# Optimization experiments

Measured on AMD Instinct MI355X. Metric: run time of the kernel, lower is better.

## Reference

```python
import jax, jax.numpy as jnp
import numpy as np

N_NODES = 100000
N_EDGES = 3200000
D_FEAT = 64


def setup_inputs() -> dict:
    key = jax.random.key(0)
    k1, k2, k3, k4 = jax.random.split(key, 4)
    features = jax.random.normal(k1, (N_NODES, D_FEAT), dtype=jnp.float32)
    vals = jax.random.uniform(k2, (N_EDGES,), dtype=jnp.float32)  # Laplacian nonzero values (e.g. 1/sqrt(di*dj))
    rows = jax.random.randint(k3, (N_EDGES,), 0, N_NODES)
    cols = jax.random.randint(k4, (N_EDGES,), 0, N_NODES)
    return {"features": features, "vals": vals, "rows": rows, "cols": cols}


def reference(features, vals, rows, cols):
    # (L + I) @ features, with L given in COO (rows, cols, vals).
    # Gather source node features, scale by edge value, scatter-add to destination rows.
    msgs = vals[:, None] * features[cols]              # [E, d]
    agg = jax.ops.segment_sum(msgs, rows, num_segments=N_NODES)  # [N, d]
    # self-loop (identity sparse matrix) fused as a direct add
    return agg + features
```

## Files before the change

kernel.cpp:

```cpp
#include <hip/hip_runtime.h>
#include <hip/hip_bf16.h>
#include <hip/hip_fp16.h>

#define D 64
#define RB 200
#define NB_MAX 512
#define MAGIC 21474944u
#define SC_BLK 256
#define TILE_T 32
#define TILE (SC_BLK * TILE_T)

__device__ __forceinline__ int bucket_of(int r) {
    return (int)__umulhi((unsigned)r, MAGIC);
}

__global__ void k_hist(const int* __restrict__ rows, int* __restrict__ counts,
                       int E, int nb) {
    __shared__ int h[NB_MAX];
    for (int i = threadIdx.x; i < nb; i += blockDim.x) h[i] = 0;
    __syncthreads();
    int i = blockIdx.x * blockDim.x + threadIdx.x;
    int stride = gridDim.x * blockDim.x;
    for (; i < E; i += stride) atomicAdd(&h[bucket_of(rows[i])], 1);
    __syncthreads();
    for (int j = threadIdx.x; j < nb; j += blockDim.x)
        if (h[j]) atomicAdd(&counts[j], h[j]);
}

__global__ void k_scan(const int* __restrict__ counts, int* __restrict__ starts,
                       int* __restrict__ cursor, int nb) {
    __shared__ int lds[NB_MAX];
    int t = threadIdx.x;
    int v = (t < nb) ? counts[t] : 0;
    lds[t] = v;
    __syncthreads();
    for (int off = 1; off < NB_MAX; off <<= 1) {
        int x = (t >= off) ? lds[t - off] : 0;
        __syncthreads();
        lds[t] += x;
        __syncthreads();
    }
    if (t < nb) {
        int excl = lds[t] - v;
        starts[t] = excl;
        cursor[t] = excl;
        if (t == nb - 1) starts[nb] = lds[t];
    }
}

__global__ void __launch_bounds__(SC_BLK) k_scatter(
    const int* __restrict__ rows, const int* __restrict__ cols,
    const float* __restrict__ vals, int* __restrict__ cursor,
    unsigned long long* __restrict__ packed1, int E, int nb) {
    __shared__ int cnt[NB_MAX];
    __shared__ int bas[NB_MAX];
    __shared__ int cnt2[NB_MAX];
    int t = threadIdx.x;
    int tile = blockIdx.x * TILE;
    for (int i = t; i < nb; i += SC_BLK) { cnt[i] = 0; cnt2[i] = 0; }
    __syncthreads();

    int rk[TILE_T];
#pragma unroll
    for (int k = 0; k < TILE_T; ++k) {
        int e = tile + k * SC_BLK + t;
        rk[k] = (e < E) ? rows[e] : -1;
        if (rk[k] >= 0) atomicAdd(&cnt[bucket_of(rk[k])], 1);
    }
    __syncthreads();
    for (int i = t; i < nb; i += SC_BLK)
        if (cnt[i]) bas[i] = atomicAdd(&cursor[i], cnt[i]);
    __syncthreads();
#pragma unroll
    for (int k = 0; k < TILE_T; ++k) {
        int e = tile + k * SC_BLK + t;
        if (rk[k] >= 0) {
            int b = bucket_of(rk[k]);
            int slot = atomicAdd(&cnt2[b], 1);
            int pos = bas[b] + slot;
            int roff = rk[k] - b * RB;
            unsigned lo = ((unsigned)roff << 17) | (unsigned)cols[e];
            packed1[pos] =
                ((unsigned long long)__float_as_uint(vals[e]) << 32) | lo;
        }
    }
}

__global__ void __launch_bounds__(1024) k_sort(
    const unsigned long long* __restrict__ packed1, const int* __restrict__ starts,
    unsigned* __restrict__ packed2, int* __restrict__ rowptr, int N, int E) {
    __shared__ int rhist[RB];
    __shared__ int rcur[RB];
    __shared__ int sc[256];
    int b = blockIdx.x;
    int t = threadIdx.x;
    int s = starts[b];
    int e = starts[b + 1];

    for (int i = t; i < RB; i += 1024) rhist[i] = 0;
    __syncthreads();
    for (int i = s + t; i < e; i += 1024) {
        unsigned lo = (unsigned)packed1[i];
        atomicAdd(&rhist[(lo >> 17) & 0xFF], 1);
    }
    __syncthreads();
    if (t < 256) sc[t] = (t < RB) ? rhist[t] : 0;
    __syncthreads();
    for (int off = 1; off < 256; off <<= 1) {
        int x = (t < 256 && t >= off) ? sc[t - off] : 0;
        __syncthreads();
        if (t < 256) sc[t] += x;
        __syncthreads();
    }
    if (t < RB) rcur[t] = sc[t] - rhist[t];
    __syncthreads();

    int gbase = b * RB;
    int nr = N - gbase; if (nr > RB) nr = RB;
    if (t < nr) rowptr[gbase + t] = s + (sc[t] - rhist[t]);
    if (b == 0 && t == 0) rowptr[N] = E;

    for (int i = s + t; i < e; i += 1024) {
        unsigned long long dj = packed1[i];
        unsigned lo = (unsigned)dj;
        int ro = (int)((lo >> 17) & 0xFF);
        int slot = atomicAdd(&rcur[ro], 1);
        float v = __uint_as_float((unsigned)(dj >> 32));
        unsigned hb = (unsigned)__half_as_ushort(__float2half(v));
        packed2[s + slot] = (hb << 17) | (lo & 0x1FFFFu);
    }
}

__global__ void __launch_bounds__(256) k_spmm(
    const float* __restrict__ feat, const unsigned* __restrict__ packed2,
    const int* __restrict__ rowptr, float* __restrict__ out, int N) {
    int lane = threadIdx.x & 63;
    int wid = (int)(((long long)blockIdx.x * blockDim.x + threadIdx.x) >> 6);
    if (wid >= N) return;
    int s = rowptr[wid];
    int e = rowptr[wid + 1];

    float acc = feat[(size_t)wid * D + lane];
    int i = s;
    for (; i + 8 <= e; i += 8) {
        float g[8], vv[8];
#pragma unroll
        for (int u = 0; u < 8; ++u) {
            unsigned d = packed2[i + u];
            vv[u] = __half2float(__ushort_as_half((unsigned short)(d >> 17)));
            g[u] = feat[(size_t)(d & 0x1FFFFu) * D + lane];
        }
#pragma unroll
        for (int u = 0; u < 8; ++u) acc = fmaf(vv[u], g[u], acc);
    }
    for (; i < e; ++i) {
        unsigned d = packed2[i];
        float v = __half2float(__ushort_as_half((unsigned short)(d >> 17)));
        acc = fmaf(v, feat[(size_t)(d & 0x1FFFFu) * D + lane], acc);
    }
    out[(size_t)wid * D + lane] = acc;
}

__global__ void gp_init_kernel(const float4* __restrict__ feat, float4* __restrict__ out,
                               int n4) {
    int i = blockIdx.x * blockDim.x + threadIdx.x;
    int stride = gridDim.x * blockDim.x;
    for (; i < n4; i += stride) out[i] = feat[i];
}
__global__ void gp_edge_kernel(const float* __restrict__ feat, const float* __restrict__ vals,
                               const int* __restrict__ rows, const int* __restrict__ cols,
                               float* __restrict__ out, int n_edges) {
    int lane = threadIdx.x & 63;
    long long gtid = (long long)blockIdx.x * blockDim.x + threadIdx.x;
    int e = (int)(gtid >> 6);
    if (e >= n_edges) return;
    int r = rows[e];
    int c = cols[e];
    float v = vals[e];
    float x = feat[(long long)c * D + lane];
    unsafeAtomicAdd(&out[(long long)r * D + lane], v * x);
}

extern "C" void kernel_launch(void* const* d_in, const int* in_sizes, int n_in,
                              void* d_out, int out_size, void* d_ws, size_t ws_size,
                              hipStream_t stream) {
    const float* feat = (const float*)d_in[0];
    const float* vals = (const float*)d_in[1];
    const int* rows = (const int*)d_in[2];
    const int* cols = (const int*)d_in[3];
    float* out = (float*)d_out;

    int E = in_sizes[1];
    int N = out_size / D;
    int nb = (N + RB - 1) / RB;

    size_t off_rowptr = (size_t)E * 4;
    size_t off_counts = off_rowptr + (size_t)(N + 1) * 4;
    size_t off_starts = off_counts + (size_t)NB_MAX * 4;
    size_t off_cursor = off_starts + (size_t)(NB_MAX + 1) * 4;
    size_t needed = off_cursor + (size_t)NB_MAX * 4;
    bool out_fits = ((size_t)out_size * 4) >= ((size_t)E * 8);

    if (ws_size >= needed && nb <= NB_MAX && N < 131072 && out_fits) {
        char* ws = (char*)d_ws;
        unsigned* packed2 = (unsigned*)ws;
        int* rowptr = (int*)(ws + off_rowptr);
        int* counts = (int*)(ws + off_counts);
        int* starts = (int*)(ws + off_starts);
        int* cursor = (int*)(ws + off_cursor);
        unsigned long long* packed1 = (unsigned long long*)d_out;

        hipMemsetAsync(counts, 0, (size_t)nb * 4, stream);
        k_hist<<<256, 256, 0, stream>>>(rows, counts, E, nb);
        k_scan<<<1, NB_MAX, 0, stream>>>(counts, starts, cursor, nb);
        int gScat = (E + TILE - 1) / TILE;
        k_scatter<<<gScat, SC_BLK, 0, stream>>>(rows, cols, vals, cursor, packed1, E, nb);
        k_sort<<<nb, 1024, 0, stream>>>(packed1, starts, packed2, rowptr, N, E);
        long long tt = (long long)N * 64;
        k_spmm<<<(int)((tt + 255) / 256), 256, 0, stream>>>(feat, packed2, rowptr, out, N);
    } else {
        int n4 = out_size / 4;
        int grid = (n4 + 255) / 256;
        if (grid > 4096) grid = 4096;
        gp_init_kernel<<<grid, 256, 0, stream>>>((const float4*)feat, (float4*)out, n4);
        long long tthreads = (long long)E * 64;
        gp_edge_kernel<<<(int)((tthreads + 255) / 256), 256, 0, stream>>>(feat, vals, rows, cols,
                                                                          out, E);
    }
}
```

Before: 317.5 us.

## Stage bucket scatter through LDS for coalesced writes and vectorize histogram loads

The scatter kernel now sorts each 4096-edge tile by bucket in shared memory, using a local prefix scan, and then writes records out contiguously per bucket. Previously each thread scattered 8-byte records directly to random global slots. The change also vectorizes the row loads in the histogram and scatter kernels with int4/float4. It adds a block-level scan, more LDS use (about 48KB per block) and extra syncs, which may reduce occupancy.

```diff
diff --git a/kernel.cpp b/kernel.cpp
--- a/kernel.cpp
+++ b/kernel.cpp
@@ -6,9 +6,8 @@
 #define RB 200
 #define NB_MAX 512
 #define MAGIC 21474944u
-#define SC_BLK 256
-#define TILE_T 32
-#define TILE (SC_BLK * TILE_T)
+#define SC_TILE 4096
+#define SC_PT 16
 
 __device__ __forceinline__ int bucket_of(int r) {
     return (int)__umulhi((unsigned)r, MAGIC);
@@ -19,9 +18,19 @@
     __shared__ int h[NB_MAX];
     for (int i = threadIdx.x; i < nb; i += blockDim.x) h[i] = 0;
     __syncthreads();
+    int E4 = E >> 2;
     int i = blockIdx.x * blockDim.x + threadIdx.x;
     int stride = gridDim.x * blockDim.x;
-    for (; i < E; i += stride) atomicAdd(&h[bucket_of(rows[i])], 1);
+    const int4* rows4 = (const int4*)rows;
+    for (; i < E4; i += stride) {
+        int4 r4 = rows4[i];
+        atomicAdd(&h[bucket_of(r4.x)], 1);
+        atomicAdd(&h[bucket_of(r4.y)], 1);
+        atomicAdd(&h[bucket_of(r4.z)], 1);
+        atomicAdd(&h[bucket_of(r4.w)], 1);
+    }
+    int t0 = E4 * 4 + blockIdx.x * blockDim.x + threadIdx.x;
+    if (t0 < E) atomicAdd(&h[bucket_of(rows[t0])], 1);
     __syncthreads();
     for (int j = threadIdx.x; j < nb; j += blockDim.x)
         if (h[j]) atomicAdd(&counts[j], h[j]);
@@ -48,42 +57,107 @@
     }
 }
 
-__global__ void __launch_bounds__(SC_BLK) k_scatter(
+__global__ void __launch_bounds__(256) k_scatter2(
     const int* __restrict__ rows, const int* __restrict__ cols,
     const float* __restrict__ vals, int* __restrict__ cursor,
-    unsigned long long* __restrict__ packed1, int E, int nb) {
+    unsigned long long* __restrict__ packed1, int E) {
+    __shared__ unsigned long long recs[SC_TILE];
+    __shared__ int dsts[SC_TILE];
     __shared__ int cnt[NB_MAX];
+    __shared__ int tst[NB_MAX];
     __shared__ int bas[NB_MAX];
-    __shared__ int cnt2[NB_MAX];
+    __shared__ int cur[NB_MAX];
+
     int t = threadIdx.x;
-    int tile = blockIdx.x * TILE;
-    for (int i = t; i < nb; i += SC_BLK) { cnt[i] = 0; cnt2[i] = 0; }
-    __syncthreads();
-
-    int rk[TILE_T];
-#pragma unroll
-    for (int k = 0; k < TILE_T; ++k) {
-        int e = tile + k * SC_BLK + t;
-        rk[k] = (e < E) ? rows[e] : -1;
-        if (rk[k] >= 0) atomicAdd(&cnt[bucket_of(rk[k])], 1);
-    }
-    __syncthreads();
-    for (int i = t; i < nb; i += SC_BLK)
-        if (cnt[i]) bas[i] = atomicAdd(&cursor[i], cnt[i]);
-    __syncthreads();
-#pragma unroll
-    for (int k = 0; k < TILE_T; ++k) {
-        int e = tile + k * SC_BLK + t;
-        if (rk[k] >= 0) {
-            int b = bucket_of(rk[k]);
-            int slot = atomicAdd(&cnt2[b], 1);
-            int pos = bas[b] + slot;
-            int roff = rk[k] - b * RB;
-            unsigned lo = ((unsigned)roff << 17) | (unsigned)cols[e];
-            packed1[pos] =
-                ((unsigned long long)__float_as_uint(vals[e]) << 32) | lo;
-        }
-    }
+    int tile = blockIdx.x * SC_TILE;
+    int tile_n = E - tile; if (tile_n > SC_TILE) tile_n = SC_TILE;
+    bool full = (tile_n == SC_TILE);
+
+    cnt[t] = 0; cnt[t + 256] = 0;
+    __syncthreads();
+
+    int r[SC_PT];
+    int e0 = tile + t * SC_PT;
+    if (full) {
+        const int4* r4 = (const int4*)(rows + e0);
+#pragma unroll
+        for (int g = 0; g < 4; ++g) {
+            int4 rr = r4[g];
+            r[g * 4 + 0] = rr.x; r[g * 4 + 1] = rr.y;
+            r[g * 4 + 2] = rr.z; r[g * 4 + 3] = rr.w;
+        }
+#pragma unroll
+        for (int u = 0; u < SC_PT; ++u) atomicAdd(&cnt[bucket_of(r[u])], 1);
+    } else {
+#pragma unroll
+        for (int u = 0; u < SC_PT; ++u) {
+            int e = e0 + u;
+            r[u] = (e < E) ? rows[e] : -1;
+            if (r[u] >= 0) atomicAdd(&cnt[bucket_of(r[u])], 1);
+        }
+    }
+    __syncthreads();
+
+    {
+        int c0 = cnt[t], c1 = cnt[t + 256];
+        bas[t] = c0 ? atomicAdd(&cursor[t], c0) : 0;
+        bas[t + 256] = c1 ? atomicAdd(&cursor[t + 256], c1) : 0;
+        tst[t] = c0; tst[t + 256] = c1;
+    }
+    __syncthreads();
+    for (int off = 1; off < NB_MAX; off <<= 1) {
+        int v0 = (t >= off) ? tst[t - off] : 0;
+        int v1 = (t + 256 >= off) ? tst[t + 256 - off] : 0;
+        __syncthreads();
+        tst[t] += v0; tst[t + 256] += v1;
+        __syncthreads();
+    }
+    {
+        int e0_ = tst[t] - cnt[t];
+        int e1_ = tst[t + 256] - cnt[t + 256];
+        __syncthreads();
+        tst[t] = e0_; tst[t + 256] = e1_;
+        cur[t] = e0_; cur[t + 256] = e1_;
+    }
+    __syncthreads();
+
+    if (full) {
+        const int4* c4 = (const int4*)(cols + e0);
+        const float4* v4 = (const float4*)(vals + e0);
+#pragma unroll
+        for (int g = 0; g < 4; ++g) {
+            int4 cc = c4[g];
+            float4 vv = v4[g];
+            int carr[4] = {cc.x, cc.y, cc.z, cc.w};
+            float varr[4] = {vv.x, vv.y, vv.z, vv.w};
+#pragma unroll
+            for (int w = 0; w < 4; ++w) {
+                int u = g * 4 + w;
+                int b = bucket_of(r[u]);
+                int slot = atomicAdd(&cur[b], 1);
+                int roff = r[u] - b * RB;
+                unsigned lo = ((unsigned)roff << 17) | (unsigned)carr[w];
+                recs[slot] = ((unsigned long long)__float_as_uint(varr[w]) << 32) | lo;
+                dsts[slot] = bas[b] + (slot - tst[b]);
+            }
+        }
+    } else {
+#pragma unroll
+        for (int u = 0; u < SC_PT; ++u) {
+            int e = e0 + u;
+            if (r[u] >= 0) {
+                int b = bucket_of(r[u]);
+                int slot = atomicAdd(&cur[b], 1);
+                int roff = r[u] - b * RB;
+                unsigned lo = ((unsigned)roff << 17) | (unsigned)cols[e];
+                recs[slot] = ((unsigned long long)__float_as_uint(vals[e]) << 32) | lo;
+                dsts[slot] = bas[b] + (slot - tst[b]);
+            }
+        }
+    }
+    __syncthreads();
+
+    for (int j = t; j < tile_n; j += 256) packed1[dsts[j]] = recs[j];
 }
 
 __global__ void __launch_bounds__(1024) k_sort(
@@ -213,8 +287,8 @@
         hipMemsetAsync(counts, 0, (size_t)nb * 4, stream);
         k_hist<<<256, 256, 0, stream>>>(rows, counts, E, nb);
         k_scan<<<1, NB_MAX, 0, stream>>>(counts, starts, cursor, nb);
-        int gScat = (E + TILE - 1) / TILE;
-        k_scatter<<<gScat, SC_BLK, 0, stream>>>(rows, cols, vals, cursor, packed1, E, nb);
+        int gScat = (E + SC_TILE - 1) / SC_TILE;
+        k_scatter2<<<gScat, 256, 0, stream>>>(rows, cols, vals, cursor, packed1, E);
         k_sort<<<nb, 1024, 0, stream>>>(packed1, starts, packed2, rowptr, N, E);
         long long tt = (long long)N * 64;
         k_spmm<<<(int)((tt + 255) / 256), 256, 0, stream>>>(feat, packed2, rowptr, out, N);
```

Result: faster. 280.0 us (-11.8%).
